# Kernel tuning notes

Hardware: AMD Instinct MI355X
Metric: run time of the kernel (lower is better)

The kernel has to match this reference:

```python
import jax, jax.numpy as jnp
import numpy as np

B, T, D_IN, H, D = 4, 4096, 1024, 16, 64


def setup_inputs() -> dict:
    key = jax.random.key(0)
    k1, k2, k3 = jax.random.split(key, 3)
    inputs = jax.random.normal(k1, (B, T, D_IN), dtype=jnp.float32)
    kv_kernel = jax.random.normal(k2, (D_IN, H, D, 2), dtype=jnp.float32) * (1.0 / np.sqrt(D_IN))
    q_kernel = jax.random.normal(k3, (H, D), dtype=jnp.float32) * (1.0 / np.sqrt(D))
    return {"inputs": inputs, "kv_kernel": kv_kernel, "q_kernel": q_kernel}


def _associate(a, b):
    # Online-softmax combine on packed tuples [m(1), u(1), w(D)] along last axis.
    ma, ua, wa = a[..., :1], a[..., 1:2], a[..., 2:]
    mb, ub, wb = b[..., :1], b[..., 1:2], b[..., 2:]
    m = jnp.maximum(ma, mb)
    ea = jnp.exp(ma - m)
    eb = jnp.exp(mb - m)
    u = ua * ea + ub * eb
    w = wa * ea + wb * eb
    return jnp.concatenate([m, u, w], axis=-1)


def reference(inputs, kv_kernel, q_kernel):
    # inputs: (B,T,D_in); kv_kernel: (D_in,H,D,2); q_kernel: (H,D)
    kv = jnp.einsum('bti,ihdk->bthdk', inputs, kv_kernel)
    kv = jax.nn.relu(kv)  # activation; dropout disabled (inference)
    k = kv[..., 0]  # (B,T,H,D)
    v = kv[..., 1]  # (B,T,H,D)
    st = jnp.einsum('hd,bthd->bth', q_kernel, k)[..., None]  # (B,T,H,1)
    u_init = jnp.ones_like(st)  # exp(s - m) with m = s
    elems = jnp.concatenate([st, u_init, v], axis=-1)  # (B,T,H,D+2)
    o = jax.lax.associative_scan(_associate, elems, axis=1)
    c = o[..., 1:2]  # running denominator
    a = o[..., 2:]   # running numerator (B,T,H,D)
    h = a / c
    # concat_heads=False -> sum over heads
    return jnp.sum(h, axis=-2)  # (B,T,D)
```

## Files before the change

kernel.cpp:

```cpp
#include <hip/hip_runtime.h>
#include <hip/hip_bf16.h>
#include <math.h>

#define B_   4
#define T_   4096
#define DIN_ 1024
#define H_   16
#define D_   64
#define M_   (B_*T_)
#define N_   (H_*D_*2)
#define K_   DIN_
#define C_   64
#define CL_  (T_/C_)

typedef unsigned short u16;
typedef __attribute__((ext_vector_type(8))) short short8_t;
typedef __attribute__((ext_vector_type(4))) float float4_t;

__device__ __forceinline__ u16 f2bf(float f) {
  unsigned int x = __float_as_uint(f);
  x += 0x7fffu + ((x >> 16) & 1u);
  return (u16)(x >> 16);
}
__device__ __forceinline__ float bf2f(unsigned int u) {
  return __uint_as_float((u & 0xffffu) << 16);
}

__device__ __forceinline__ void g2l16(const u16* g, u16* l) {
  __builtin_amdgcn_global_load_lds(
      (const __attribute__((address_space(1))) void*)g,
      (__attribute__((address_space(3))) void*)l, 16, 0, 0);
}

__global__ __launch_bounds__(256)
void prep(const float* __restrict__ inputs, const float* __restrict__ kvk,
          u16* __restrict__ aB, u16* __restrict__ wBt) {
  __shared__ float tile[32][33];
  int bid = blockIdx.x;
  int tid = threadIdx.x;
  if (bid < 8192) {
    int i = bid * 256 + tid;
    const float4* src = (const float4*)inputs;
    float4 a = src[2*i], b = src[2*i+1];
    uint4 o;
    o.x = (unsigned)f2bf(a.x) | ((unsigned)f2bf(a.y) << 16);
    o.y = (unsigned)f2bf(a.z) | ((unsigned)f2bf(a.w) << 16);
    o.z = (unsigned)f2bf(b.x) | ((unsigned)f2bf(b.y) << 16);
    o.w = (unsigned)f2bf(b.z) | ((unsigned)f2bf(b.w) << 16);
    ((uint4*)aB)[i] = o;
  } else {
    int b2 = bid - 8192;
    int kb = (b2 & 31) * 32;
    int nb = (b2 >> 5) * 32;
    int r  = tid >> 3;
    int c4 = (tid & 7) * 4;
    float4 v = *(const float4*)&kvk[(size_t)(kb + r) * N_ + nb + c4];
    tile[r][c4+0] = v.x; tile[r][c4+1] = v.y; tile[r][c4+2] = v.z; tile[r][c4+3] = v.w;
    __syncthreads();
    unsigned lo = (unsigned)f2bf(tile[c4+0][r]) | ((unsigned)f2bf(tile[c4+1][r]) << 16);
    unsigned hi = (unsigned)f2bf(tile[c4+2][r]) | ((unsigned)f2bf(tile[c4+3][r]) << 16);
    uint2 o; o.x = lo; o.y = hi;
    *(uint2*)&wBt[(size_t)(nb + r) * K_ + kb + c4] = o;
  }
}

__global__ __launch_bounds__(256)
void gemm_kv(const u16* __restrict__ A, const u16* __restrict__ Bt,
             const float* __restrict__ q,
             float* __restrict__ sbuf, u16* __restrict__ vbuf,
             float* __restrict__ aggM, float* __restrict__ aggU,
             float* __restrict__ aggW) {
  __shared__ __align__(16) char smem[33536];
  u16*   vtile = (u16*)smem;
  float* sred  = (float*)(smem + 18432);
  float* qs    = (float*)(smem + 32768);
  float* sS    = (float*)(smem + 33024);

  const int tid  = threadIdx.x;
  const int wave = tid >> 6;
  const int lane = tid & 63;
  const int quad = lane >> 4;
  const int l16  = lane & 15;

  const int g    = blockIdx.x;
  const int xcd  = g & 7;
  const int slot = g >> 3;
  const int h    = slot & 15;
  const int mt   = (slot >> 4) * 8 + xcd;
  const int bm = mt * 128;
  const int bn = h * 128;
  const int wm = (wave >> 1) * 64;
  const int wn = (wave & 1) * 64;

  if (tid < D_) qs[tid] = q[h * D_ + tid];

  const int r4 = lane >> 2;
  const int cc = lane & 3;
  const int gk = ((cc ^ ((r4 >> 1) & 3))) * 8;
  const u16* ga0 = A  + (size_t)(bm + wave*16 + r4) * K_ + gk;
  const u16* ga1 = ga0 + (size_t)64 * K_;
  const u16* gb0 = Bt + (size_t)(bn + wave*16 + r4) * K_ + gk;
  const u16* gb1 = gb0 + (size_t)64 * K_;
  const int laOff = (wave*16) * 32;
  const int lbOff = (wave*16) * 32;

  const int swz = (quad ^ ((l16 >> 1) & 3)) * 8;

  float4_t acc[4][4] = {};

  {
    u16* lA0 = (u16*)smem;
    u16* lB0 = (u16*)(smem + 8192);
    g2l16(ga0, lA0 + laOff);
    g2l16(ga1, lA0 + laOff + 64*32);
    g2l16(gb0, lB0 + lbOff);
    g2l16(gb1, lB0 + lbOff + 64*32);
  }

  for (int it = 0; it < 32; ++it) {
    u16* lAc = (u16*)(smem + (it & 1) * 16384);
    u16* lBc = (u16*)(smem + (it & 1) * 16384 + 8192);
    __syncthreads();
    if (it < 31) {
      int kn = (it + 1) * 32;
      u16* lAn = (u16*)(smem + ((it + 1) & 1) * 16384);
      u16* lBn = (u16*)(smem + ((it + 1) & 1) * 16384 + 8192);
      g2l16(ga0 + kn, lAn + laOff);
      g2l16(ga1 + kn, lAn + laOff + 64*32);
      g2l16(gb0 + kn, lBn + lbOff);
      g2l16(gb1 + kn, lBn + lbOff + 64*32);
    }

    short8_t af[4], bfr[4];
#pragma unroll
    for (int i = 0; i < 4; ++i)
      af[i] = *(const short8_t*)&lAc[(wm + i*16 + l16) * 32 + swz];
#pragma unroll
    for (int j = 0; j < 4; ++j)
      bfr[j] = *(const short8_t*)&lBc[(wn + j*16 + l16) * 32 + swz];
#pragma unroll
    for (int i = 0; i < 4; ++i)
#pragma unroll
      for (int j = 0; j < 4; ++j)
        acc[i][j] = __builtin_amdgcn_mfma_f32_16x16x32_bf16(af[i], bfr[j], acc[i][j], 0, 0, 0);
  }

  __syncthreads();

  if (l16 & 1) {
#pragma unroll
    for (int j = 0; j < 4; ++j) {
      int d = ((wn + j*16 + l16) & 127) >> 1;
#pragma unroll
      for (int i = 0; i < 4; ++i)
#pragma unroll
        for (int r = 0; r < 4; ++r) {
          int t = wm + i*16 + quad*4 + r;
          vtile[t*72 + d] = f2bf(fmaxf(acc[i][j][r], 0.f));
        }
    }
  } else {
    int slot2 = (wn >> 3) + (l16 >> 1);
#pragma unroll
    for (int i = 0; i < 4; ++i)
#pragma unroll
      for (int r = 0; r < 4; ++r) {
        int t = wm + i*16 + quad*4 + r;
        float p = 0.f;
#pragma unroll
        for (int j = 0; j < 4; ++j) {
          int d = ((wn + j*16 + l16) & 127) >> 1;
          p += qs[d] * fmaxf(acc[i][j][r], 0.f);
        }
        sred[t*17 + slot2] = p;
      }
  }
  __syncthreads();

  const int b   = mt >> 5;
  const int tt0 = (mt & 31) * 128;
  const int bh  = b * H_ + h;

  if (tid < 128) {
    float ssum = 0.f;
#pragma unroll
    for (int k = 0; k < 16; ++k) ssum += sred[tid*17 + k];
    sS[tid] = ssum;
    sbuf[(size_t)bh * T_ + tt0 + tid] = ssum;
  }
  __syncthreads();

  if (wave < 2) {
    int d = lane;
    float m = -INFINITY, u = 0.f, w = 0.f;
#pragma unroll 4
    for (int i = 0; i < CL_; ++i) {
      int t = wave * CL_ + i;
      float si = sS[t];
      float v  = bf2f(vtile[t*72 + d]);
      float mn    = fmaxf(m, si);
      float alpha = __expf(m - mn);
      float p     = __expf(si - mn);
      u = u * alpha + p;
      w = w * alpha + p * v;
      m = mn;
    }
    int blk = bh * C_ + (mt & 31) * 2 + wave;
    aggW[(size_t)blk * D_ + d] = w;
    if (d == 0) { aggM[blk] = m; aggU[blk] = u; }
  } else {
    int idx = tid - 128;
    int d0  = (idx & 7) * 8;
    int tr  = idx >> 3;
    u16* vg = vbuf + ((size_t)bh * T_ + tt0) * D_;
#pragma unroll
    for (int itv = 0; itv < 8; ++itv) {
      int t = tr + 16*itv;
      uint4 val = *(const uint4*)&vtile[t*72 + d0];
      *(uint4*)&vg[(size_t)t * D_ + d0] = val;
    }
  }
}

__global__ __launch_bounds__(1024)
void scan_pass3(const u16* __restrict__ vbuf, const float* __restrict__ sbuf,
                const float* __restrict__ aggM, const float* __restrict__ aggU,
                const float* __restrict__ aggW, float* __restrict__ out) {
  __shared__ float sS[H_][CL_];
  __shared__ float wbuf[H_][8][D_ + 1];
  int bc = blockIdx.x;
  int b  = bc >> 6;
  int c  = bc & (C_ - 1);
  int tid  = threadIdx.x;
  int h    = tid >> 6;
  int lane = tid & 63;
  int bh   = b * H_ + h;
  int t0   = c * CL_;

  sS[h][lane] = sbuf[(size_t)bh * T_ + t0 + lane];

  float m = -INFINITY, u = 0.f, w = 0.f;
  for (int j = 0; j < c; ++j) {
    int idx = bh * C_ + j;
    float Mc = aggM[idx];
    float Uc = aggU[idx];
    float Wc = aggW[(size_t)idx * D_ + lane];
    float mn = fmaxf(m, Mc);
    float ea = __expf(m - mn);
    float eb = __expf(Mc - mn);
    u = u * ea + Uc * eb;
    w = w * ea + Wc * eb;
    m = mn;
  }
  __syncthreads();

  const u16* vp = vbuf + ((size_t)bh * T_ + t0) * D_ + lane;
  for (int gg = 0; gg < 8; ++gg) {
#pragma unroll
    for (int ii = 0; ii < 8; ++ii) {
      int i = gg * 8 + ii;
      float si = sS[h][i];
      float v  = bf2f(vp[i * D_]);
      float mn    = fmaxf(m, si);
      float alpha = __expf(m - mn);
      float p     = __expf(si - mn);
      u = u * alpha + p;
      w = w * alpha + p * v;
      m = mn;
      wbuf[h][ii][lane] = __fdividef(w, u);
    }
    __syncthreads();
    if (tid < 512) {
      int ii = tid >> 6, dd = tid & 63;
      float acc = 0.f;
#pragma unroll
      for (int hh = 0; hh < H_; ++hh) acc += wbuf[hh][ii][dd];
      out[((size_t)b * T_ + t0 + gg*8 + ii) * D_ + dd] = acc;
    }
    __syncthreads();
  }
}

extern "C" void kernel_launch(void* const* d_in, const int* in_sizes, int n_in,
                              void* d_out, int out_size, void* d_ws, size_t ws_size,
                              hipStream_t stream) {
  const float* inputs = (const float*)d_in[0];
  const float* kvk    = (const float*)d_in[1];
  const float* qk     = (const float*)d_in[2];
  float* out = (float*)d_out;
  char* ws = (char*)d_ws;

  u16*   aB   = (u16*)ws;
  u16*   wBt  = (u16*)(ws + 33554432);
  u16*   vb   = (u16*)(ws + 37748736);
  float* sb   = (float*)(ws + 71303168);
  float* aggM = (float*)(ws + 72351744);
  float* aggU = (float*)(ws + 72368128);
  float* aggW = (float*)(ws + 72384512);

  prep<<<10240, 256, 0, stream>>>(inputs, kvk, aB, wBt);
  gemm_kv<<<2048, 256, 0, stream>>>(aB, wBt, qk, sb, vb, aggM, aggU, aggW);
  scan_pass3<<<B_*C_, 1024, 0, stream>>>(vb, sb, aggM, aggU, aggW, out);
}
```

Baseline: 239.7 us.

## Switch GEMM main loop to single-buffered BK=64 tiles with XOR swizzle

Replaces the double-buffered K=32 loop, which prefetched the next tile while computing the current one, with a single-buffered K=64 loop that loads, syncs, then computes. The LDS layout moves to 64-wide rows with an 8-way XOR swizzle, so each iteration issues twice as many MFMAs per barrier pair and runs half as many iterations. The trade-off is that global-to-LDS loads are no longer overlapped with MFMA work inside a block, and latency hiding now depends on other resident blocks.

```diff
diff --git a/kernel.cpp b/kernel.cpp
--- a/kernel.cpp
+++ b/kernel.cpp
@@ -71,6 +71,8 @@
              float* __restrict__ aggM, float* __restrict__ aggU,
              float* __restrict__ aggW) {
   __shared__ __align__(16) char smem[33536];
+  u16*   lA    = (u16*)smem;
+  u16*   lB    = (u16*)(smem + 16384);
   u16*   vtile = (u16*)smem;
   float* sred  = (float*)(smem + 18432);
   float* qs    = (float*)(smem + 32768);
@@ -94,55 +96,46 @@
 
   if (tid < D_) qs[tid] = q[h * D_ + tid];
 
-  const int r4 = lane >> 2;
-  const int cc = lane & 3;
-  const int gk = ((cc ^ ((r4 >> 1) & 3))) * 8;
-  const u16* ga0 = A  + (size_t)(bm + wave*16 + r4) * K_ + gk;
-  const u16* ga1 = ga0 + (size_t)64 * K_;
-  const u16* gb0 = Bt + (size_t)(bn + wave*16 + r4) * K_ + gk;
-  const u16* gb1 = gb0 + (size_t)64 * K_;
-  const int laOff = (wave*16) * 32;
-  const int lbOff = (wave*16) * 32;
-
-  const int swz = (quad ^ ((l16 >> 1) & 3)) * 8;
+  const int r8 = lane >> 3;
+  const int k8 = lane & 7;
+  const int gk = (k8 ^ r8) * 8;
+  const u16* gaBase = A  + (size_t)(bm + wave*32 + r8) * K_ + gk;
+  const u16* gbBase = Bt + (size_t)(bn + wave*32 + r8) * K_ + gk;
+
+  const int fs0 = ((quad    ) ^ (l16 & 7)) * 8;
+  const int fs1 = ((quad + 4) ^ (l16 & 7)) * 8;
 
   float4_t acc[4][4] = {};
 
-  {
-    u16* lA0 = (u16*)smem;
-    u16* lB0 = (u16*)(smem + 8192);
-    g2l16(ga0, lA0 + laOff);
-    g2l16(ga1, lA0 + laOff + 64*32);
-    g2l16(gb0, lB0 + lbOff);
-    g2l16(gb1, lB0 + lbOff + 64*32);
-  }
-
-  for (int it = 0; it < 32; ++it) {
-    u16* lAc = (u16*)(smem + (it & 1) * 16384);
-    u16* lBc = (u16*)(smem + (it & 1) * 16384 + 8192);
-    __syncthreads();
-    if (it < 31) {
-      int kn = (it + 1) * 32;
-      u16* lAn = (u16*)(smem + ((it + 1) & 1) * 16384);
-      u16* lBn = (u16*)(smem + ((it + 1) & 1) * 16384 + 8192);
-      g2l16(ga0 + kn, lAn + laOff);
-      g2l16(ga1 + kn, lAn + laOff + 64*32);
-      g2l16(gb0 + kn, lBn + lbOff);
-      g2l16(gb1 + kn, lBn + lbOff + 64*32);
-    }
-
-    short8_t af[4], bfr[4];
-#pragma unroll
-    for (int i = 0; i < 4; ++i)
-      af[i] = *(const short8_t*)&lAc[(wm + i*16 + l16) * 32 + swz];
-#pragma unroll
-    for (int j = 0; j < 4; ++j)
-      bfr[j] = *(const short8_t*)&lBc[(wn + j*16 + l16) * 32 + swz];
-#pragma unroll
-    for (int i = 0; i < 4; ++i)
-#pragma unroll
-      for (int j = 0; j < 4; ++j)
-        acc[i][j] = __builtin_amdgcn_mfma_f32_16x16x32_bf16(af[i], bfr[j], acc[i][j], 0, 0, 0);
+  for (int k0 = 0; k0 < K_; k0 += 64) {
+    __syncthreads();
+#pragma unroll
+    for (int call = 0; call < 4; ++call) {
+      g2l16(gaBase + k0 + (size_t)(call*8) * K_, lA + (wave*32 + call*8) * 64);
+      g2l16(gbBase + k0 + (size_t)(call*8) * K_, lB + (wave*32 + call*8) * 64);
+    }
+    __syncthreads();
+
+    short8_t af[4][2], bfr[4][2];
+#pragma unroll
+    for (int i = 0; i < 4; ++i) {
+      int row = (wm + i*16 + l16) * 64;
+      af[i][0] = *(const short8_t*)&lA[row + fs0];
+      af[i][1] = *(const short8_t*)&lA[row + fs1];
+    }
+#pragma unroll
+    for (int j = 0; j < 4; ++j) {
+      int row = (wn + j*16 + l16) * 64;
+      bfr[j][0] = *(const short8_t*)&lB[row + fs0];
+      bfr[j][1] = *(const short8_t*)&lB[row + fs1];
+    }
+#pragma unroll
+    for (int t = 0; t < 2; ++t)
+#pragma unroll
+      for (int i = 0; i < 4; ++i)
+#pragma unroll
+        for (int j = 0; j < 4; ++j)
+          acc[i][j] = __builtin_amdgcn_mfma_f32_16x16x32_bf16(af[i][t], bfr[j][t], acc[i][j], 0, 0, 0);
   }
 
   __syncthreads();
```

New measurement: 228.5 us. 1.05x faster.
